# Optimization experiments

Measured on AMD Instinct MI355X. Metric: run time of the kernel, lower is better.

Reference implementation:

```python
import jax, jax.numpy as jnp
import numpy as np

N = 100000          # total nodes
E = 3200000         # total edges (avg degree 32)
B = 100             # num graphs
NPG = N // B        # nodes per graph (uniform -> to_dense_batch is a reshape)
D_IN, D_H, D_E, N_CLS = 128, 64, 32, 10


def setup_inputs() -> dict:
    key = jax.random.key(0)
    ks = jax.random.split(key, 12)
    x = jax.random.normal(ks[0], (N, D_IN), jnp.float32)
    # edges strictly within each graph: offset by graph block
    epg = E // B
    offs = (jnp.arange(E, dtype=jnp.int32) // epg) * NPG
    src = jax.random.randint(ks[1], (E,), 0, NPG, jnp.int32) + offs
    dst = jax.random.randint(ks[2], (E,), 0, NPG, jnp.int32) + offs
    edge_index = jnp.stack([src, dst])
    batch = jnp.repeat(jnp.arange(B, dtype=jnp.int32), NPG)

    def glorot(k, fi, fo):
        return jax.random.normal(k, (fi, fo), jnp.float32) * (1.0 / np.sqrt(fi))

    return {
        "x": x, "edge_index": edge_index, "batch": batch,
        "W_a1": glorot(ks[3], D_IN, D_H), "b_a1": jnp.zeros((D_H,), jnp.float32),
        "W_a2": glorot(ks[4], D_H, D_E),  "b_a2": jnp.zeros((D_E,), jnp.float32),
        "W_x1": glorot(ks[5], D_IN, D_H), "b_x1": jnp.zeros((D_H,), jnp.float32),
        "W_x2": glorot(ks[6], D_H, D_E),  "b_x2": jnp.zeros((D_E,), jnp.float32),
        "W_lin": glorot(ks[7], D_E * D_E, N_CLS),
        "b_lin": jnp.zeros((N_CLS,), jnp.float32),
    }


def _gcn(x, W, b, src, dst, n):
    """PyG GCNConv(improved=True): sym-norm with self-loop weight 2."""
    h = x @ W                                                   # [n, out]
    deg = jax.ops.segment_sum(jnp.ones_like(dst, h.dtype), dst, n) + 2.0
    dinv = jax.lax.rsqrt(deg)                                   # [n]
    coef = dinv[src] * dinv[dst]                                # [E]
    agg = jax.ops.segment_sum(h[src] * coef[:, None], dst, n)   # gather-scatter
    agg = agg + (2.0 * dinv * dinv)[:, None] * h                # self-loop term
    return agg + b


def _segment_softmax(v, seg, nseg):
    m = jax.ops.segment_max(v, seg, nseg)
    e = jnp.exp(v - m[seg])
    s = jax.ops.segment_sum(e, seg, nseg)
    return e / s[seg]


def reference(x, edge_index, batch, W_a1, b_a1, W_a2, b_a2,
              W_x1, b_x1, W_x2, b_x2, W_lin, b_lin):
    src, dst = edge_index[0], edge_index[1]
    n = x.shape[0]
    a1 = jax.nn.relu(_gcn(x, W_a1, b_a1, src, dst, n))
    a2 = _segment_softmax(_gcn(a1, W_a2, b_a2, src, dst, n), batch, B)
    x1 = jax.nn.relu(_gcn(x, W_x1, b_x1, src, dst, n))
    x2 = jax.nn.relu(_gcn(x1, W_x2, b_x2, src, dst, n))
    # uniform graph sizes -> to_dense_batch is a reshape (no padding needed)
    a_b = a2.reshape(B, NPG, D_E)
    x_b = x2.reshape(B, NPG, D_E)
    prods = jnp.einsum('bne,bnf->bef', a_b, x_b)   # bmm(a^T, x): [B, D_E, D_E]
    flat = prods.reshape(B, D_E * D_E)
    return jax.nn.softmax(flat @ W_lin + b_lin, axis=-1)
```

## Files before the change

### kernel.cpp

```cpp
#include <hip/hip_runtime.h>
#include <hip/hip_bf16.h>
#include <hip/hip_fp16.h>

#define N_NODES 100000
#define N_EDGES 3200000
#define NB      100
#define NPG     1000
#define EPG     32000
#define DIN     128
#define DH      64
#define DE      32
#define NCLS    10
#define CNT_BLOCKS  832
#define SORT_BLOCKS 416


typedef _Float16 h2_t __attribute__((ext_vector_type(2)));
typedef _Float16 h8_t __attribute__((ext_vector_type(8)));
typedef float    f4_t __attribute__((ext_vector_type(4)));

__device__ __forceinline__ float dot2f(unsigned a, unsigned b, float c) {
#if __has_builtin(__builtin_amdgcn_fdot2)
    return __builtin_amdgcn_fdot2(__builtin_bit_cast(h2_t, a),
                                  __builtin_bit_cast(h2_t, b), c, false);
#else
    float d;
    asm("v_dot2_f32_f16 %0, %1, %2, %3" : "=v"(d) : "v"(a), "v"(b), "v"(c));
    return d;
#endif
}

#define DOT8(rA, rB, dv)                                                        \
    acc[0] = dot2f(__builtin_amdgcn_perm(rB.x, rA.x, 0x05040100u), dv, acc[0]); \
    acc[1] = dot2f(__builtin_amdgcn_perm(rB.x, rA.x, 0x07060302u), dv, acc[1]); \
    acc[2] = dot2f(__builtin_amdgcn_perm(rB.y, rA.y, 0x05040100u), dv, acc[2]); \
    acc[3] = dot2f(__builtin_amdgcn_perm(rB.y, rA.y, 0x07060302u), dv, acc[3]); \
    acc[4] = dot2f(__builtin_amdgcn_perm(rB.z, rA.z, 0x05040100u), dv, acc[4]); \
    acc[5] = dot2f(__builtin_amdgcn_perm(rB.z, rA.z, 0x07060302u), dv, acc[5]); \
    acc[6] = dot2f(__builtin_amdgcn_perm(rB.w, rA.w, 0x05040100u), dv, acc[6]); \
    acc[7] = dot2f(__builtin_amdgcn_perm(rB.w, rA.w, 0x07060302u), dv, acc[7]);

__device__ __forceinline__ unsigned fenc(float f) {
    unsigned u = __float_as_uint(f);
    return u ^ (unsigned)(((int)u >> 31) | (int)0x80000000);
}
__device__ __forceinline__ float fdec(unsigned key) {
    return (key & 0x80000000u) ? __uint_as_float(key ^ 0x80000000u)
                               : __uint_as_float(~key);
}


__global__ __launch_bounds__(256) void k_cnt(const int* __restrict__ dst,
                                             int* __restrict__ cnt8) {
    __shared__ int cnt[NPG];
    int slice = blockIdx.x >> 3;
    int g = (blockIdx.x & 7) + 8 * (slice % 13);
    int sub = slice / 13;
    if (g >= NB) return;
    int t = threadIdx.x;
    for (int i = t; i < NPG; i += 256) cnt[i] = 0;
    __syncthreads();
    int ebase = g * EPG + sub * 4000, nbase = g * NPG;
    for (int i = t; i < 4000; i += 256)
        atomicAdd(&cnt[dst[ebase + i] - nbase], 1);
    __syncthreads();
    for (int i = t; i < NPG; i += 256)
        cnt8[sub * N_NODES + nbase + i] = cnt[i];
}


__global__ __launch_bounds__(1024) void k_scan(const int* __restrict__ cnt8,
                                               int* __restrict__ rowptr,
                                               float* __restrict__ dinv,
                                               unsigned short* __restrict__ dh16) {
    __shared__ int sm[1024];
    int g = (blockIdx.x & 7) + 8 * (blockIdx.x >> 3);
    if (g >= NB) return;
    int t = threadIdx.x;
    int nbase = g * NPG, ebase = g * EPG;
    int v = 0;
    if (t < NPG) {
        #pragma unroll
        for (int s8 = 0; s8 < 8; s8++) v += cnt8[s8 * N_NODES + nbase + t];
        float dv = rsqrtf((float)v + 2.0f);
        dinv[nbase + t] = dv;
        dh16[nbase + t] = __half_as_ushort(__float2half_rn(dv));
    }
    sm[t] = v;
    __syncthreads();
    for (int off = 1; off < 1024; off <<= 1) {
        int xx = (t >= off) ? sm[t - off] : 0;
        __syncthreads();
        sm[t] += xx;
        __syncthreads();
    }
    if (t < NPG)
        rowptr[nbase + t] = ebase + sm[t] - v;
    if (g == NB - 1 && t == 0) rowptr[N_NODES] = N_EDGES;
}


union SharedSG {
    struct {
        int cur[256];
        unsigned buf[10000];
    } sc;
    struct {
        __align__(16) unsigned short wt[16384];
    } ge;
};

__global__ __launch_bounds__(1024) void k_sg(const int* __restrict__ src,
                                             const int* __restrict__ dst,
                                             const float* __restrict__ x,
                                             const float* __restrict__ Wa,
                                             const float* __restrict__ Wx,
                                             const int* __restrict__ rowptr,
                                             const unsigned short* __restrict__ dh16,
                                             unsigned int* __restrict__ esrc,
                                             unsigned short* __restrict__ h16) {
    __shared__ SharedSG S;
    int t = threadIdx.x;
    if (blockIdx.x < SORT_BLOCKS) {
        int xcd = blockIdx.x & 7, slot = blockIdx.x >> 3;
        int g = xcd + 8 * (slot % 13);
        int q = slot / 13;
        if (g >= NB) return;
        int nbase = g * NPG, ebase = g * EPG;
        int n0 = q * 250;
        int base0 = rowptr[nbase + n0];
        int cap = rowptr[nbase + n0 + 250] - base0;
        if (t < 250)
            S.sc.cur[t] = rowptr[nbase + n0 + t] - base0;
        __syncthreads();
        for (int i = t; i < EPG; i += 1024) {
            int d = dst[ebase + i] - nbase - n0;
            if ((unsigned)d < 250u) {
                int s = src[ebase + i];
                int pos = atomicAdd(&S.sc.cur[d], 1);
                S.sc.buf[pos] = ((unsigned)(s - nbase) * 16) |
                                ((unsigned)dh16[s] << 16);
            }
        }
        __syncthreads();
        for (int i = t; i < cap; i += 1024)
            esrc[base0 + i] = S.sc.buf[i];
    } else {
        int b2 = blockIdx.x - SORT_BLOCKS;
        int xcd = b2 & 7, slot = b2 >> 3;
        int g = xcd + 8 * (slot >> 2);
        int chunk = slot & 3;
        if (g >= NB) return;
        int row0 = g * NPG + chunk * 250;
        {
            int cc = t & 127, kg = t >> 7;
            const float* Wp = (cc < 64) ? &Wa[cc] : &Wx[cc - 64];
            #pragma unroll
            for (int j = 0; j < 4; j++) {
                int k0 = kg * 16 + j * 4;
                union { __half h[4]; uint2 u; } pk;
                #pragma unroll
                for (int m = 0; m < 4; m++)
                    pk.h[m] = __float2half_rn(Wp[(k0 + m) * 64]);
                int byte = cc * 256 + ((2 * k0) ^ ((cc & 7) << 4));
                *(uint2*)((char*)S.ge.wt + byte) = pk.u;
            }
        }
        __syncthreads();
        int w = t >> 6, l = t & 63;
        int lr = l & 15, kq = l >> 4;
        int rowA = row0 + w * 16 + lr;
        int rA = rowA < N_NODES ? rowA : N_NODES - 1;
        const float* xr = &x[(size_t)rA * 128];
        h8_t a[4];
        #pragma unroll
        for (int kc = 0; kc < 4; kc++) {
            float4 lo = *(const float4*)&xr[kc * 32 + kq * 8];
            float4 hi = *(const float4*)&xr[kc * 32 + kq * 8 + 4];
            h8_t av;
            av[0] = (_Float16)lo.x; av[1] = (_Float16)lo.y;
            av[2] = (_Float16)lo.z; av[3] = (_Float16)lo.w;
            av[4] = (_Float16)hi.x; av[5] = (_Float16)hi.y;
            av[6] = (_Float16)hi.z; av[7] = (_Float16)hi.w;
            a[kc] = av;
        }
        f4_t acc[8] = {};
        #pragma unroll
        for (int kc = 0; kc < 4; kc++) {
            #pragma unroll
            for (int n = 0; n < 8; n++) {
                int cc = n * 16 + lr;
                int byte = cc * 256 + (((kc * 32 + kq * 8) * 2) ^ ((cc & 7) << 4));
                h8_t bf = *(h8_t*)((char*)S.ge.wt + byte);
                acc[n] = __builtin_amdgcn_mfma_f32_16x16x32_f16(a[kc], bf, acc[n], 0, 0, 0);
            }
        }
        int rowD = row0 + w * 16 + kq * 4;
        #pragma unroll
        for (int n = 0; n < 8; n++) {
            #pragma unroll
            for (int j = 0; j < 4; j++) {
                int r = rowD + j;
                if (r < N_NODES)
                    h16[(size_t)r * 128 + n * 16 + lr] =
                        __half_as_ushort(__float2half_rn(acc[n][j]));
            }
        }
    }
}


__global__ __launch_bounds__(256) void k_agg128(const unsigned short* __restrict__ h16,
                                                const int* __restrict__ rowptr,
                                                const unsigned int* __restrict__ esrc,
                                                const float* __restrict__ dinv,
                                                const float* __restrict__ ba,
                                                const float* __restrict__ bx,
                                                unsigned short* __restrict__ outB16) {
    int xcd = blockIdx.x & 7, slot = blockIdx.x >> 3;
    int gi = slot / 63, chunk = slot - gi * 63;
    int g = xcd + 8 * gi;
    if (g >= NB) return;
    int grp = threadIdx.x >> 4;
    int cl  = threadIdx.x & 15;
    int nl  = chunk * 16 + grp;
    int valid = nl < NPG;
    int nlc = valid ? nl : NPG - 1;
    int wid = g * NPG + nlc;
    const uint4* hg4 = (const uint4*)(h16 + (size_t)g * NPG * 128);
    float acc[8] = {};
    union U8 { uint4 u; __half h[8]; };
    int e0 = rowptr[wid];
    int e1 = valid ? rowptr[wid + 1] : e0;
    int e = e0;
    for (; e + 8 <= e1; e += 8) {
        unsigned pv0 = esrc[e + 0], pv1 = esrc[e + 1];
        unsigned pv2 = esrc[e + 2], pv3 = esrc[e + 3];
        unsigned pv4 = esrc[e + 4], pv5 = esrc[e + 5];
        unsigned pv6 = esrc[e + 6], pv7 = esrc[e + 7];
        uint4 r0 = hg4[(pv0 & 0xffffu) + cl];
        uint4 r1 = hg4[(pv1 & 0xffffu) + cl];
        uint4 r2 = hg4[(pv2 & 0xffffu) + cl];
        uint4 r3 = hg4[(pv3 & 0xffffu) + cl];
        uint4 r4 = hg4[(pv4 & 0xffffu) + cl];
        uint4 r5 = hg4[(pv5 & 0xffffu) + cl];
        uint4 r6 = hg4[(pv6 & 0xffffu) + cl];
        uint4 r7 = hg4[(pv7 & 0xffffu) + cl];
        unsigned dA = __builtin_amdgcn_perm(pv1, pv0, 0x07060302u);
        unsigned dB = __builtin_amdgcn_perm(pv3, pv2, 0x07060302u);
        unsigned dC = __builtin_amdgcn_perm(pv5, pv4, 0x07060302u);
        unsigned dD = __builtin_amdgcn_perm(pv7, pv6, 0x07060302u);
        DOT8(r0, r1, dA);
        DOT8(r2, r3, dB);
        DOT8(r4, r5, dC);
        DOT8(r6, r7, dD);
    }
    for (; e + 2 <= e1; e += 2) {
        unsigned pv0 = esrc[e], pv1 = esrc[e + 1];
        uint4 r0 = hg4[(pv0 & 0xffffu) + cl];
        uint4 r1 = hg4[(pv1 & 0xffffu) + cl];
        unsigned dA = __builtin_amdgcn_perm(pv1, pv0, 0x07060302u);
        DOT8(r0, r1, dA);
    }
    if (e < e1) {
        unsigned pv = esrc[e];
        uint4 r = hg4[(pv & 0xffffu) + cl];
        unsigned dA = pv >> 16;
        DOT8(r, r, dA);
    }
    float di = dinv[wid];
    float sw = 2.0f * di * di;
    U8 hv; hv.u = hg4[nlc * 16 + cl];
    int cl8 = cl * 8;
    const float* bb = (cl8 < 64) ? &ba[cl8] : &bx[cl8 - 64];
    union { __half2 h2[4]; uint4 q; } pk;
    #pragma unroll
    for (int k = 0; k < 4; k++) {
        float ox = fmaxf(di * acc[2 * k]     + sw * __half2float(hv.h[2 * k])     + bb[2 * k],     0.0f);
        float oy = fmaxf(di * acc[2 * k + 1] + sw * __half2float(hv.h[2 * k + 1]) + bb[2 * k + 1], 0.0f);
        pk.h2[k] = __floats2half2_rn(ox, oy);
    }
    if (valid)
        *(uint4*)&outB16[(size_t)wid * 128 + cl8] = pk.q;
}


__global__ __launch_bounds__(256) void k_agg64(const unsigned short* __restrict__ g16,
                                               const int* __restrict__ rowptr,
                                               const unsigned int* __restrict__ esrc,
                                               const float* __restrict__ dinv,
                                               const float* __restrict__ ba2,
                                               const float* __restrict__ bx2,
                                               float* __restrict__ s2,
                                               float* __restrict__ pmax) {
    __shared__ unsigned pm[32];
    int xcd = blockIdx.x & 7, slot = blockIdx.x >> 3;
    int gi = slot >> 5, chunk = slot & 31;
    int g = xcd + 8 * gi;
    if (g >= NB) return;
    int t = threadIdx.x;
    if (t < 32) pm[t] = 0u;
    __syncthreads();
    int grp = t >> 3;
    int cl  = t & 7;
    int nl  = chunk * 32 + grp;
    int valid = nl < NPG;
    int nlc = valid ? nl : NPG - 1;
    int wid = g * NPG + nlc;
    const uint4* gg4 = (const uint4*)(g16 + (size_t)g * NPG * 64);
    float acc[8] = {};
    union U8 { uint4 u; __half h[8]; };
    int e0 = rowptr[wid];
    int e1 = valid ? rowptr[wid + 1] : e0;
    int e = e0;
    for (; e + 8 <= e1; e += 8) {
        unsigned pv0 = esrc[e + 0], pv1 = esrc[e + 1];
        unsigned pv2 = esrc[e + 2], pv3 = esrc[e + 3];
        unsigned pv4 = esrc[e + 4], pv5 = esrc[e + 5];
        unsigned pv6 = esrc[e + 6], pv7 = esrc[e + 7];
        uint4 r0 = gg4[((pv0 & 0xffffu) >> 1) + cl];
        uint4 r1 = gg4[((pv1 & 0xffffu) >> 1) + cl];
        uint4 r2 = gg4[((pv2 & 0xffffu) >> 1) + cl];
        uint4 r3 = gg4[((pv3 & 0xffffu) >> 1) + cl];
        uint4 r4 = gg4[((pv4 & 0xffffu) >> 1) + cl];
        uint4 r5 = gg4[((pv5 & 0xffffu) >> 1) + cl];
        uint4 r6 = gg4[((pv6 & 0xffffu) >> 1) + cl];
        uint4 r7 = gg4[((pv7 & 0xffffu) >> 1) + cl];
        unsigned dA = __builtin_amdgcn_perm(pv1, pv0, 0x07060302u);
        unsigned dB = __builtin_amdgcn_perm(pv3, pv2, 0x07060302u);
        unsigned dC = __builtin_amdgcn_perm(pv5, pv4, 0x07060302u);
        unsigned dD = __builtin_amdgcn_perm(pv7, pv6, 0x07060302u);
        DOT8(r0, r1, dA);
        DOT8(r2, r3, dB);
        DOT8(r4, r5, dC);
        DOT8(r6, r7, dD);
    }
    for (; e + 2 <= e1; e += 2) {
        unsigned pv0 = esrc[e], pv1 = esrc[e + 1];
        uint4 r0 = gg4[((pv0 & 0xffffu) >> 1) + cl];
        uint4 r1 = gg4[((pv1 & 0xffffu) >> 1) + cl];
        unsigned dA = __builtin_amdgcn_perm(pv1, pv0, 0x07060302u);
        DOT8(r0, r1, dA);
    }
    if (e < e1) {
        unsigned pv = esrc[e];
        uint4 r = gg4[((pv & 0xffffu) >> 1) + cl];
        unsigned dA = pv >> 16;
        DOT8(r, r, dA);
    }
    float di = dinv[wid];
    float sw = 2.0f * di * di;
    U8 hv; hv.u = gg4[nlc * 8 + cl];
    int cl8 = cl * 8;
    float o[8];
    #pragma unroll
    for (int k = 0; k < 8; k++)
        o[k] = di * acc[k] + sw * __half2float(hv.h[k]);
    if (cl8 < 32) {
        #pragma unroll
        for (int k = 0; k < 8; k++) o[k] += ba2[cl8 + k];
    } else {
        #pragma unroll
        for (int k = 0; k < 8; k++) o[k] = fmaxf(o[k] + bx2[cl8 - 32 + k], 0.0f);
    }
    if (valid) {
        *(float4*)&s2[(size_t)wid * 64 + cl8]     = make_float4(o[0], o[1], o[2], o[3]);
        *(float4*)&s2[(size_t)wid * 64 + cl8 + 4] = make_float4(o[4], o[5], o[6], o[7]);
    }
    if (valid && cl < 4) {
        #pragma unroll
        for (int k = 0; k < 8; k++)
            atomicMax(&pm[cl8 + k], fenc(o[k]));
    }
    __syncthreads();
    if (t < 32)
        pmax[((size_t)g * 32 + chunk) * 32 + t] = fdec(pm[t]);
}


__global__ __launch_bounds__(256) void k_gemm2(const unsigned short* __restrict__ Bm16,
                                               const float* __restrict__ Wa2,
                                               const float* __restrict__ Wx2,
                                               unsigned short* __restrict__ g16) {
    __shared__ __align__(16) unsigned short wt2[8192];
    int xcd = blockIdx.x & 7, slot = blockIdx.x >> 3;
    int g = xcd + 8 * (slot >> 4);
    int chunk = slot & 15;
    if (g >= NB) return;
    int row0 = g * NPG + chunk * 64;
    int t = threadIdx.x;
    {
        int cc = t & 63, kg = t >> 6;
        #pragma unroll
        for (int j = 0; j < 8; j++) {
            int k0 = kg * 32 + j * 4;
            union { __half h[4]; uint2 u; } pk;
            #pragma unroll
            for (int m = 0; m < 4; m++) {
                int k = k0 + m;
                float v;
                if (cc < 32) v = (k < 64)  ? Wa2[k * 32 + cc] : 0.0f;
                else         v = (k >= 64) ? Wx2[(k - 64) * 32 + (cc - 32)] : 0.0f;
                pk.h[m] = __float2half_rn(v);
            }
            int byte = cc * 256 + ((2 * k0) ^ ((cc & 7) << 4));
            *(uint2*)((char*)wt2 + byte) = pk.u;
        }
    }
    __syncthreads();
    int w = t >> 6, l = t & 63;
    int lr = l & 15, kq = l >> 4;
    int rowA = row0 + w * 16 + lr;
    int rA = rowA < N_NODES ? rowA : N_NODES - 1;
    const unsigned short* xr = &Bm16[(size_t)rA * 128];
    h8_t a[4];
    #pragma unroll
    for (int kc = 0; kc < 4; kc++)
        a[kc] = *(const h8_t*)&xr[kc * 32 + kq * 8];
    f4_t acc[4] = {};
    #pragma unroll
    for (int kc = 0; kc < 4; kc++) {
        #pragma unroll
        for (int n = 0; n < 4; n++) {
            int cc = n * 16 + lr;
            int byte = cc * 256 + (((kc * 32 + kq * 8) * 2) ^ ((cc & 7) << 4));
            h8_t bf = *(h8_t*)((char*)wt2 + byte);
            acc[n] = __builtin_amdgcn_mfma_f32_16x16x32_f16(a[kc], bf, acc[n], 0, 0, 0);
        }
    }
    int rowD = row0 + w * 16 + kq * 4;
    #pragma unroll
    for (int n = 0; n < 4; n++) {
        #pragma unroll
        for (int j = 0; j < 4; j++) {
            int r = rowD + j;
            if (r < N_NODES)
                g16[(size_t)r * 64 + n * 16 + lr] =
                    __half_as_ushort(__float2half_rn(acc[n][j]));
        }
    }
}


__global__ __launch_bounds__(256) void k_pool(const float* __restrict__ s2,
                                              const float* __restrict__ pmax,
                                              float* __restrict__ psum,
                                              float* __restrict__ prods) {
    __shared__ float ta[25][32];
    __shared__ float tx[25][32];
    __shared__ float gm[32];
    int xcd = blockIdx.x & 7, slot = blockIdx.x >> 3;
    int g = xcd + 8 * (slot >> 3);
    int ch = slot & 7;
    if (g >= NB) return;
    int t = threadIdx.x;
    if (t < 32) {
        float m = -1e30f;
        for (int j = 0; j < 32; j++)
            m = fmaxf(m, pmax[((size_t)g * 32 + j) * 32 + t]);
        gm[t] = m;
    }
    int e  = t >> 3;
    int f4 = t & 7;
    float a0 = 0.f, a1 = 0.f, a2 = 0.f, a3 = 0.f;
    float csum = 0.f;
    int base = g * NPG + ch * 125;
    for (int n0 = 0; n0 < 125; n0 += 25) {
        __syncthreads();
        for (int i = t; i < 25 * 16; i += 256) {
            int r = i >> 4, c4 = i & 15;
            float4 v = *(const float4*)&s2[(size_t)(base + n0 + r) * 64 + c4 * 4];
            if (c4 < 8) {
                int cb = c4 * 4;
                v.x = __expf(v.x - gm[cb + 0]);
                v.y = __expf(v.y - gm[cb + 1]);
                v.z = __expf(v.z - gm[cb + 2]);
                v.w = __expf(v.w - gm[cb + 3]);
                *(float4*)&ta[r][cb] = v;
            } else {
                *(float4*)&tx[r][(c4 - 8) * 4] = v;
            }
        }
        __syncthreads();
        if (t < 32) {
            #pragma unroll 5
            for (int r = 0; r < 25; r++) csum += ta[r][t];
        }
        #pragma unroll 5
        for (int n = 0; n < 25; n++) {
            float a   = ta[n][e];
            float4 xv = *(float4*)&tx[n][f4 * 4];
            a0 += a * xv.x; a1 += a * xv.y; a2 += a * xv.z; a3 += a * xv.w;
        }
    }
    if (t < 32)
        psum[((size_t)g * 8 + ch) * 32 + t] = csum;
    *(float4*)&prods[((size_t)(g * 8 + ch)) * 1024 + e * 32 + f4 * 4] =
        make_float4(a0, a1, a2, a3);
}


__global__ __launch_bounds__(256) void k_head(const float* __restrict__ prods,
                                              const float* __restrict__ psum,
                                              const float* __restrict__ Wlin,
                                              const float* __restrict__ blin,
                                              float* __restrict__ out) {
    __shared__ float red[4][NCLS];
    __shared__ float sinvv[32];
    int g = (blockIdx.x & 7) + 8 * (blockIdx.x >> 3);
    if (g >= NB) return;
    int t = threadIdx.x;
    if (t < 32) {
        float s = 0.f;
        for (int q = 0; q < 8; q++) s += psum[((size_t)g * 8 + q) * 32 + t];
        sinvv[t] = 1.0f / s;
    }
    __syncthreads();
    float p[NCLS];
    for (int c = 0; c < NCLS; c++) p[c] = 0.0f;
    const float* pg = &prods[(size_t)g * 8 * 1024];
    for (int j = 0; j < 4; j++) {
        int k = t * 4 + j;
        int e = k >> 5;
        float v = 0.0f;
        #pragma unroll
        for (int q = 0; q < 8; q++) v += pg[q * 1024 + k];
        v *= sinvv[e];
        const float* wrow = &Wlin[k * NCLS];
        for (int c = 0; c < NCLS; c++) p[c] += v * wrow[c];
    }
    for (int off = 32; off > 0; off >>= 1)
        for (int c = 0; c < NCLS; c++) p[c] += __shfl_down(p[c], off, 64);
    int wave = t >> 6, lane = t & 63;
    if (lane == 0)
        for (int c = 0; c < NCLS; c++) red[wave][c] = p[c];
    __syncthreads();
    if (t == 0) {
        float logits[NCLS]; float mx = -1e30f;
        for (int c = 0; c < NCLS; c++) {
            logits[c] = red[0][c] + red[1][c] + red[2][c] + red[3][c] + blin[c];
            mx = fmaxf(mx, logits[c]);
        }
        float s = 0.0f;
        for (int c = 0; c < NCLS; c++) { logits[c] = expf(logits[c] - mx); s += logits[c]; }
        float inv = 1.0f / s;
        for (int c = 0; c < NCLS; c++) out[g * NCLS + c] = logits[c] * inv;
    }
}


extern "C" void kernel_launch(void* const* d_in, const int* in_sizes, int n_in,
                              void* d_out, int out_size, void* d_ws, size_t ws_size,
                              hipStream_t stream) {
    const float* x    = (const float*)d_in[0];
    const int*   ei   = (const int*)d_in[1];
    const float* Wa1  = (const float*)d_in[3];
    const float* ba1  = (const float*)d_in[4];
    const float* Wa2  = (const float*)d_in[5];
    const float* ba2  = (const float*)d_in[6];
    const float* Wx1  = (const float*)d_in[7];
    const float* bx1  = (const float*)d_in[8];
    const float* Wx2  = (const float*)d_in[9];
    const float* bx2  = (const float*)d_in[10];
    const float* Wlin = (const float*)d_in[11];
    const float* blin = (const float*)d_in[12];
    float* out = (float*)d_out;

    char* w = (char*)d_ws;
    auto alloc = [&](size_t bytes) -> void* {
        void* p = (void*)w;
        w += (bytes + 255) & ~(size_t)255;
        return p;
    };
    int*            rowptr = (int*)alloc((N_NODES + 1) * sizeof(int));
    int*            cnt8   = (int*)alloc((size_t)8 * N_NODES * sizeof(int));
    float*          dinv   = (float*)alloc(N_NODES * sizeof(float));
    unsigned short* dh16   = (unsigned short*)alloc(N_NODES * sizeof(unsigned short));
    unsigned int*   esrc   = (unsigned int*)alloc((size_t)N_EDGES * sizeof(unsigned int));
    float*          pmax   = (float*)alloc((size_t)NB * 32 * 32 * sizeof(float));
    float*          psum   = (float*)alloc((size_t)NB * 8 * 32 * sizeof(float));
    float*          prods  = (float*)alloc((size_t)NB * 8 * 1024 * sizeof(float));
    unsigned short* h16    = (unsigned short*)alloc((size_t)N_NODES * 128 * sizeof(unsigned short));
    unsigned short* b16    = (unsigned short*)alloc((size_t)N_NODES * 128 * sizeof(unsigned short));
    unsigned short* g16    = (unsigned short*)alloc((size_t)N_NODES * 64 * sizeof(unsigned short));
    float*          s2     = (float*)alloc((size_t)N_NODES * 64 * sizeof(float));

    const int* srcp = ei;
    const int* dstp = ei + N_EDGES;

    k_cnt<<<CNT_BLOCKS, 256, 0, stream>>>(dstp, cnt8);
    k_scan<<<8 * 13, 1024, 0, stream>>>(cnt8, rowptr, dinv, dh16);
    k_sg<<<SORT_BLOCKS + 8 * 13 * 4, 1024, 0, stream>>>(srcp, dstp, x, Wa1, Wx1,
                                                        rowptr, dh16, esrc, h16);
    k_agg128<<<8 * 13 * 63, 256, 0, stream>>>(h16, rowptr, esrc, dinv, ba1, bx1, b16);
    k_gemm2<<<8 * 13 * 16, 256, 0, stream>>>(b16, Wa2, Wx2, g16);
    k_agg64<<<8 * 13 * 32, 256, 0, stream>>>(g16, rowptr, esrc, dinv, ba2, bx2, s2, pmax);
    k_pool<<<8 * 13 * 8, 256, 0, stream>>>(s2, pmax, psum, prods);
    k_head<<<8 * 13, 256, 0, stream>>>(prods, psum, Wlin, blin, out);
}
```

Before: 288.4 us.

## Replace first-layer gather aggregation with dense per-graph SpMM on MFMA

Stores the first-layer projected features transposed per graph (channel-major). It replaces the per-node edge gather with a kernel that builds a dense 64x128 fp16 adjacency tile in shared memory for each K-slice of source nodes, then multiplies it with the feature tile using MFMA. The aim is to swap irregular gathered loads for dense tensor-core work, since each graph has only 1000 nodes. In exchange, every block rescans its edge lists 8 times, the adjacency accumulates in fp16, and the epilogue makes strided scalar reads and writes.

```diff
diff --git a/kernel.cpp b/kernel.cpp
--- a/kernel.cpp
+++ b/kernel.cpp
@@ -118,7 +118,7 @@
                                              const int* __restrict__ rowptr,
                                              const unsigned short* __restrict__ dh16,
                                              unsigned int* __restrict__ esrc,
-                                             unsigned short* __restrict__ h16) {
+                                             unsigned short* __restrict__ h16t) {
     __shared__ SharedSG S;
     int t = threadIdx.x;
     if (blockIdx.x < SORT_BLOCKS) {
@@ -195,93 +195,125 @@
                 acc[n] = __builtin_amdgcn_mfma_f32_16x16x32_f16(a[kc], bf, acc[n], 0, 0, 0);
             }
         }
-        int rowD = row0 + w * 16 + kq * 4;
+        int nodeLoc = chunk * 250 + w * 16 + kq * 4;
         #pragma unroll
         for (int n = 0; n < 8; n++) {
+            int ch = n * 16 + lr;
+            unsigned short* hrow = h16t + ((size_t)g * 128 + ch) * 1000;
             #pragma unroll
             for (int j = 0; j < 4; j++) {
-                int r = rowD + j;
-                if (r < N_NODES)
-                    h16[(size_t)r * 128 + n * 16 + lr] =
-                        __half_as_ushort(__float2half_rn(acc[n][j]));
-            }
-        }
-    }
-}
-
-
-__global__ __launch_bounds__(256) void k_agg128(const unsigned short* __restrict__ h16,
-                                                const int* __restrict__ rowptr,
-                                                const unsigned int* __restrict__ esrc,
-                                                const float* __restrict__ dinv,
-                                                const float* __restrict__ ba,
-                                                const float* __restrict__ bx,
-                                                unsigned short* __restrict__ outB16) {
+                int nl = nodeLoc + j;
+                if (nl < NPG)
+                    hrow[nl] = __half_as_ushort(__float2half_rn(acc[n][j]));
+            }
+        }
+    }
+}
+
+
+__global__ __launch_bounds__(256) void k_spmm128(const unsigned short* __restrict__ h16t,
+                                                 const int* __restrict__ rowptr,
+                                                 const unsigned int* __restrict__ esrc,
+                                                 const float* __restrict__ dinv,
+                                                 const float* __restrict__ ba,
+                                                 const float* __restrict__ bx,
+                                                 unsigned short* __restrict__ outB16) {
+    __shared__ __align__(16) unsigned short As[8192];
+    __shared__ __align__(16) unsigned short Bt[16384];
     int xcd = blockIdx.x & 7, slot = blockIdx.x >> 3;
-    int gi = slot / 63, chunk = slot - gi * 63;
+    int gi = slot >> 4, chunk = slot & 15;
     int g = xcd + 8 * gi;
     if (g >= NB) return;
-    int grp = threadIdx.x >> 4;
-    int cl  = threadIdx.x & 15;
-    int nl  = chunk * 16 + grp;
-    int valid = nl < NPG;
-    int nlc = valid ? nl : NPG - 1;
-    int wid = g * NPG + nlc;
-    const uint4* hg4 = (const uint4*)(h16 + (size_t)g * NPG * 128);
-    float acc[8] = {};
-    union U8 { uint4 u; __half h[8]; };
-    int e0 = rowptr[wid];
-    int e1 = valid ? rowptr[wid + 1] : e0;
-    int e = e0;
-    for (; e + 8 <= e1; e += 8) {
-        unsigned pv0 = esrc[e + 0], pv1 = esrc[e + 1];
-        unsigned pv2 = esrc[e + 2], pv3 = esrc[e + 3];
-        unsigned pv4 = esrc[e + 4], pv5 = esrc[e + 5];
-        unsigned pv6 = esrc[e + 6], pv7 = esrc[e + 7];
-        uint4 r0 = hg4[(pv0 & 0xffffu) + cl];
-        uint4 r1 = hg4[(pv1 & 0xffffu) + cl];
-        uint4 r2 = hg4[(pv2 & 0xffffu) + cl];
-        uint4 r3 = hg4[(pv3 & 0xffffu) + cl];
-        uint4 r4 = hg4[(pv4 & 0xffffu) + cl];
-        uint4 r5 = hg4[(pv5 & 0xffffu) + cl];
-        uint4 r6 = hg4[(pv6 & 0xffffu) + cl];
-        uint4 r7 = hg4[(pv7 & 0xffffu) + cl];
-        unsigned dA = __builtin_amdgcn_perm(pv1, pv0, 0x07060302u);
-        unsigned dB = __builtin_amdgcn_perm(pv3, pv2, 0x07060302u);
-        unsigned dC = __builtin_amdgcn_perm(pv5, pv4, 0x07060302u);
-        unsigned dD = __builtin_amdgcn_perm(pv7, pv6, 0x07060302u);
-        DOT8(r0, r1, dA);
-        DOT8(r2, r3, dB);
-        DOT8(r4, r5, dC);
-        DOT8(r6, r7, dD);
-    }
-    for (; e + 2 <= e1; e += 2) {
-        unsigned pv0 = esrc[e], pv1 = esrc[e + 1];
-        uint4 r0 = hg4[(pv0 & 0xffffu) + cl];
-        uint4 r1 = hg4[(pv1 & 0xffffu) + cl];
-        unsigned dA = __builtin_amdgcn_perm(pv1, pv0, 0x07060302u);
-        DOT8(r0, r1, dA);
-    }
-    if (e < e1) {
-        unsigned pv = esrc[e];
-        uint4 r = hg4[(pv & 0xffffu) + cl];
-        unsigned dA = pv >> 16;
-        DOT8(r, r, dA);
-    }
-    float di = dinv[wid];
-    float sw = 2.0f * di * di;
-    U8 hv; hv.u = hg4[nlc * 16 + cl];
-    int cl8 = cl * 8;
-    const float* bb = (cl8 < 64) ? &ba[cl8] : &bx[cl8 - 64];
-    union { __half2 h2[4]; uint4 q; } pk;
+    int t = threadIdx.x;
+    int w = t >> 6, l = t & 63, lr = l & 15, kq = l >> 4;
+    int n0 = chunk * 64;
+    int eb0 = 0, eb1 = 0;
+    if (t < 64) {
+        int nl = n0 + t;
+        if (nl < NPG) {
+            int wid = g * NPG + nl;
+            eb0 = rowptr[wid];
+            eb1 = rowptr[wid + 1];
+        }
+    }
+    const unsigned short* hb = h16t + (size_t)g * 128 * 1000;
+    f4_t acc[8] = {};
+    for (int sk = 0; sk < 8; sk++) {
+        __syncthreads();
+        {
+            uint4 z = make_uint4(0, 0, 0, 0);
+            #pragma unroll
+            for (int i = 0; i < 4; i++)
+                *(uint4*)((char*)As + t * 64 + i * 16) = z;
+        }
+        {
+            int tch = t >> 1, th = t & 1;
+            #pragma unroll
+            for (int i = 0; i < 8; i++) {
+                int kl = th * 64 + i * 8;
+                int nb = sk * 128 + kl;
+                int nsrc = (nb + 8 <= NPG) ? nb : (NPG - 8);
+                uint4 v = *(const uint4*)(hb + (size_t)tch * 1000 + nsrc);
+                *(uint4*)((char*)Bt + tch * 256 + ((2 * kl) ^ ((tch & 7) << 4))) = v;
+            }
+        }
+        __syncthreads();
+        if (t < 64) {
+            int slo = sk << 7;
+            int e = eb0;
+            for (; e + 4 <= eb1; e += 4) {
+                unsigned q0 = esrc[e], q1 = esrc[e + 1];
+                unsigned q2 = esrc[e + 2], q3 = esrc[e + 3];
+                #pragma unroll
+                for (int j = 0; j < 4; j++) {
+                    unsigned rec = (j == 0) ? q0 : (j == 1) ? q1 : (j == 2) ? q2 : q3;
+                    int sl = (int)((rec & 0xffffu) >> 4) - slo;
+                    if ((unsigned)sl < 128u) {
+                        __half* ap = (__half*)((char*)As + t * 256 + ((2 * sl) ^ ((t & 7) << 4)));
+                        *ap = __hadd(*ap, __ushort_as_half((unsigned short)(rec >> 16)));
+                    }
+                }
+            }
+            for (; e < eb1; e++) {
+                unsigned rec = esrc[e];
+                int sl = (int)((rec & 0xffffu) >> 4) - slo;
+                if ((unsigned)sl < 128u) {
+                    __half* ap = (__half*)((char*)As + t * 256 + ((2 * sl) ^ ((t & 7) << 4)));
+                    *ap = __hadd(*ap, __ushort_as_half((unsigned short)(rec >> 16)));
+                }
+            }
+        }
+        __syncthreads();
+        #pragma unroll
+        for (int kk = 0; kk < 4; kk++) {
+            int row = w * 16 + lr;
+            h8_t a = *(h8_t*)((char*)As + row * 256 + ((kk * 64 + kq * 16) ^ ((row & 7) << 4)));
+            #pragma unroll
+            for (int n = 0; n < 8; n++) {
+                int ch = n * 16 + lr;
+                h8_t b = *(h8_t*)((char*)Bt + ch * 256 + ((kk * 64 + kq * 16) ^ ((ch & 7) << 4)));
+                acc[n] = __builtin_amdgcn_mfma_f32_16x16x32_f16(a, b, acc[n], 0, 0, 0);
+            }
+        }
+    }
+    int nodeBase = n0 + w * 16 + kq * 4;
     #pragma unroll
-    for (int k = 0; k < 4; k++) {
-        float ox = fmaxf(di * acc[2 * k]     + sw * __half2float(hv.h[2 * k])     + bb[2 * k],     0.0f);
-        float oy = fmaxf(di * acc[2 * k + 1] + sw * __half2float(hv.h[2 * k + 1]) + bb[2 * k + 1], 0.0f);
-        pk.h2[k] = __floats2half2_rn(ox, oy);
-    }
-    if (valid)
-        *(uint4*)&outB16[(size_t)wid * 128 + cl8] = pk.q;
+    for (int j = 0; j < 4; j++) {
+        int nl = nodeBase + j;
+        if (nl < NPG) {
+            int wid = g * NPG + nl;
+            float di = dinv[wid];
+            float sw = 2.0f * di * di;
+            #pragma unroll
+            for (int n = 0; n < 8; n++) {
+                int ch = n * 16 + lr;
+                float hs = __half2float(__ushort_as_half(hb[(size_t)ch * 1000 + nl]));
+                float bbv = (ch < 64) ? ba[ch] : bx[ch - 64];
+                float o = fmaxf(di * acc[n][j] + sw * hs + bbv, 0.0f);
+                outB16[(size_t)wid * 128 + ch] = __half_as_ushort(__float2half_rn(o));
+            }
+        }
+    }
 }
 
 
@@ -580,7 +612,7 @@
     float*          pmax   = (float*)alloc((size_t)NB * 32 * 32 * sizeof(float));
     float*          psum   = (float*)alloc((size_t)NB * 8 * 32 * sizeof(float));
     float*          prods  = (float*)alloc((size_t)NB * 8 * 1024 * sizeof(float));
-    unsigned short* h16    = (unsigned short*)alloc((size_t)N_NODES * 128 * sizeof(unsigned short));
+    unsigned short* h16t   = (unsigned short*)alloc((size_t)N_NODES * 128 * sizeof(unsigned short));
     unsigned short* b16    = (unsigned short*)alloc((size_t)N_NODES * 128 * sizeof(unsigned short));
     unsigned short* g16    = (unsigned short*)alloc((size_t)N_NODES * 64 * sizeof(unsigned short));
     float*          s2     = (float*)alloc((size_t)N_NODES * 64 * sizeof(float));
@@ -591,8 +623,8 @@
     k_cnt<<<CNT_BLOCKS, 256, 0, stream>>>(dstp, cnt8);
     k_scan<<<8 * 13, 1024, 0, stream>>>(cnt8, rowptr, dinv, dh16);
     k_sg<<<SORT_BLOCKS + 8 * 13 * 4, 1024, 0, stream>>>(srcp, dstp, x, Wa1, Wx1,
-                                                        rowptr, dh16, esrc, h16);
-    k_agg128<<<8 * 13 * 63, 256, 0, stream>>>(h16, rowptr, esrc, dinv, ba1, bx1, b16);
+                                                        rowptr, dh16, esrc, h16t);
+    k_spmm128<<<8 * 13 * 16, 256, 0, stream>>>(h16t, rowptr, esrc, dinv, ba1, bx1, b16);
     k_gemm2<<<8 * 13 * 16, 256, 0, stream>>>(b16, Wa2, Wx2, g16);
     k_agg64<<<8 * 13 * 32, 256, 0, stream>>>(g16, rowptr, esrc, dinv, ba2, bx2, s2, pmax);
     k_pool<<<8 * 13 * 8, 256, 0, stream>>>(s2, pmax, psum, prods);
```

Measured after the change: 434.0 us. 1.5x slower.

## Fuse second-layer GEMM into first aggregation kernel via shared-memory MFMA

Applied to the files above, without the earlier changes.

The layer-2 weight multiply (128->64 block-diagonal) now happens inside k_agg128. Each block stages its 16 aggregated rows in swizzled LDS and runs MFMA against the fp16 weights, also staged in LDS, then writes g16 directly. This removes the k_gemm2 launch and the write and re-read of the 25.6 MB b16 intermediate. In exchange, every one of the ~6500 blocks now converts the full weight matrix to fp16 in LDS, and LDS use and the extra barrier may lower occupancy of the latency-bound gather kernel.

```diff
diff --git a/kernel.cpp b/kernel.cpp
--- a/kernel.cpp
+++ b/kernel.cpp
@@ -216,13 +216,36 @@
                                                 const float* __restrict__ dinv,
                                                 const float* __restrict__ ba,
                                                 const float* __restrict__ bx,
-                                                unsigned short* __restrict__ outB16) {
+                                                const float* __restrict__ Wa2,
+                                                const float* __restrict__ Wx2,
+                                                unsigned short* __restrict__ g16) {
+    __shared__ __align__(16) unsigned short wt2[8192];
+    __shared__ __align__(16) unsigned short bs[2048];
     int xcd = blockIdx.x & 7, slot = blockIdx.x >> 3;
     int gi = slot / 63, chunk = slot - gi * 63;
     int g = xcd + 8 * gi;
     if (g >= NB) return;
-    int grp = threadIdx.x >> 4;
-    int cl  = threadIdx.x & 15;
+    int t = threadIdx.x;
+    {
+        int cc = t & 63, kg = t >> 6;
+        #pragma unroll
+        for (int j = 0; j < 8; j++) {
+            int k0 = kg * 32 + j * 4;
+            union { __half h[4]; uint2 u; } pk;
+            #pragma unroll
+            for (int m = 0; m < 4; m++) {
+                int k = k0 + m;
+                float v;
+                if (cc < 32) v = (k < 64)  ? Wa2[k * 32 + cc] : 0.0f;
+                else         v = (k >= 64) ? Wx2[(k - 64) * 32 + (cc - 32)] : 0.0f;
+                pk.h[m] = __float2half_rn(v);
+            }
+            int byte = cc * 256 + ((2 * k0) ^ ((cc & 7) << 4));
+            *(uint2*)((char*)wt2 + byte) = pk.u;
+        }
+    }
+    int grp = t >> 4;
+    int cl  = t & 15;
     int nl  = chunk * 16 + grp;
     int valid = nl < NPG;
     int nlc = valid ? nl : NPG - 1;
@@ -268,20 +291,41 @@
         unsigned dA = pv >> 16;
         DOT8(r, r, dA);
     }
-    float di = dinv[wid];
-    float sw = 2.0f * di * di;
-    U8 hv; hv.u = hg4[nlc * 16 + cl];
-    int cl8 = cl * 8;
-    const float* bb = (cl8 < 64) ? &ba[cl8] : &bx[cl8 - 64];
-    union { __half2 h2[4]; uint4 q; } pk;
-    #pragma unroll
-    for (int k = 0; k < 4; k++) {
-        float ox = fmaxf(di * acc[2 * k]     + sw * __half2float(hv.h[2 * k])     + bb[2 * k],     0.0f);
-        float oy = fmaxf(di * acc[2 * k + 1] + sw * __half2float(hv.h[2 * k + 1]) + bb[2 * k + 1], 0.0f);
-        pk.h2[k] = __floats2half2_rn(ox, oy);
-    }
-    if (valid)
-        *(uint4*)&outB16[(size_t)wid * 128 + cl8] = pk.q;
+    {
+        float di = dinv[wid];
+        float sw = 2.0f * di * di;
+        U8 hv; hv.u = hg4[nlc * 16 + cl];
+        int cl8 = cl * 8;
+        const float* bb = (cl8 < 64) ? &ba[cl8] : &bx[cl8 - 64];
+        union { __half h[8]; uint4 q; } pk;
+        #pragma unroll
+        for (int k = 0; k < 8; k++) {
+            float o = fmaxf(di * acc[k] + sw * __half2float(hv.h[k]) + bb[k], 0.0f);
+            pk.h[k] = valid ? __float2half_rn(o) : __float2half_rn(0.0f);
+        }
+        *(uint4*)((char*)bs + grp * 256 + ((cl * 16) ^ ((grp & 7) << 4))) = pk.q;
+    }
+    __syncthreads();
+    {
+        int w = t >> 6, l = t & 63;
+        int lr = l & 15, kq = l >> 4;
+        f4_t acc2 = {0.0f, 0.0f, 0.0f, 0.0f};
+        #pragma unroll
+        for (int kc = 0; kc < 4; kc++) {
+            int kb = (kc * 32 + kq * 8) * 2;
+            h8_t a = *(h8_t*)((char*)bs + lr * 256 + (kb ^ ((lr & 7) << 4)));
+            int cc = w * 16 + lr;
+            h8_t bfr = *(h8_t*)((char*)wt2 + cc * 256 + (kb ^ ((cc & 7) << 4)));
+            acc2 = __builtin_amdgcn_mfma_f32_16x16x32_f16(a, bfr, acc2, 0, 0, 0);
+        }
+        #pragma unroll
+        for (int j = 0; j < 4; j++) {
+            int nl2 = chunk * 16 + 4 * kq + j;
+            if (nl2 < NPG)
+                g16[((size_t)(g * NPG + nl2)) * 64 + w * 16 + lr] =
+                    __half_as_ushort(__float2half_rn(acc2[j]));
+        }
+    }
 }
 
 
@@ -378,70 +422,6 @@
 }
 
 
-__global__ __launch_bounds__(256) void k_gemm2(const unsigned short* __restrict__ Bm16,
-                                               const float* __restrict__ Wa2,
-                                               const float* __restrict__ Wx2,
-                                               unsigned short* __restrict__ g16) {
-    __shared__ __align__(16) unsigned short wt2[8192];
-    int xcd = blockIdx.x & 7, slot = blockIdx.x >> 3;
-    int g = xcd + 8 * (slot >> 4);
-    int chunk = slot & 15;
-    if (g >= NB) return;
-    int row0 = g * NPG + chunk * 64;
-    int t = threadIdx.x;
-    {
-        int cc = t & 63, kg = t >> 6;
-        #pragma unroll
-        for (int j = 0; j < 8; j++) {
-            int k0 = kg * 32 + j * 4;
-            union { __half h[4]; uint2 u; } pk;
-            #pragma unroll
-            for (int m = 0; m < 4; m++) {
-                int k = k0 + m;
-                float v;
-                if (cc < 32) v = (k < 64)  ? Wa2[k * 32 + cc] : 0.0f;
-                else         v = (k >= 64) ? Wx2[(k - 64) * 32 + (cc - 32)] : 0.0f;
-                pk.h[m] = __float2half_rn(v);
-            }
-            int byte = cc * 256 + ((2 * k0) ^ ((cc & 7) << 4));
-            *(uint2*)((char*)wt2 + byte) = pk.u;
-        }
-    }
-    __syncthreads();
-    int w = t >> 6, l = t & 63;
-    int lr = l & 15, kq = l >> 4;
-    int rowA = row0 + w * 16 + lr;
-    int rA = rowA < N_NODES ? rowA : N_NODES - 1;
-    const unsigned short* xr = &Bm16[(size_t)rA * 128];
-    h8_t a[4];
-    #pragma unroll
-    for (int kc = 0; kc < 4; kc++)
-        a[kc] = *(const h8_t*)&xr[kc * 32 + kq * 8];
-    f4_t acc[4] = {};
-    #pragma unroll
-    for (int kc = 0; kc < 4; kc++) {
-        #pragma unroll
-        for (int n = 0; n < 4; n++) {
-            int cc = n * 16 + lr;
-            int byte = cc * 256 + (((kc * 32 + kq * 8) * 2) ^ ((cc & 7) << 4));
-            h8_t bf = *(h8_t*)((char*)wt2 + byte);
-            acc[n] = __builtin_amdgcn_mfma_f32_16x16x32_f16(a[kc], bf, acc[n], 0, 0, 0);
-        }
-    }
-    int rowD = row0 + w * 16 + kq * 4;
-    #pragma unroll
-    for (int n = 0; n < 4; n++) {
-        #pragma unroll
-        for (int j = 0; j < 4; j++) {
-            int r = rowD + j;
-            if (r < N_NODES)
-                g16[(size_t)r * 64 + n * 16 + lr] =
-                    __half_as_ushort(__float2half_rn(acc[n][j]));
-        }
-    }
-}
-
-
 __global__ __launch_bounds__(256) void k_pool(const float* __restrict__ s2,
                                               const float* __restrict__ pmax,
                                               float* __restrict__ psum,
@@ -581,7 +561,6 @@
     float*          psum   = (float*)alloc((size_t)NB * 8 * 32 * sizeof(float));
     float*          prods  = (float*)alloc((size_t)NB * 8 * 1024 * sizeof(float));
     unsigned short* h16    = (unsigned short*)alloc((size_t)N_NODES * 128 * sizeof(unsigned short));
-    unsigned short* b16    = (unsigned short*)alloc((size_t)N_NODES * 128 * sizeof(unsigned short));
     unsigned short* g16    = (unsigned short*)alloc((size_t)N_NODES * 64 * sizeof(unsigned short));
     float*          s2     = (float*)alloc((size_t)N_NODES * 64 * sizeof(float));
 
@@ -592,8 +571,8 @@
     k_scan<<<8 * 13, 1024, 0, stream>>>(cnt8, rowptr, dinv, dh16);
     k_sg<<<SORT_BLOCKS + 8 * 13 * 4, 1024, 0, stream>>>(srcp, dstp, x, Wa1, Wx1,
                                                         rowptr, dh16, esrc, h16);
-    k_agg128<<<8 * 13 * 63, 256, 0, stream>>>(h16, rowptr, esrc, dinv, ba1, bx1, b16);
-    k_gemm2<<<8 * 13 * 16, 256, 0, stream>>>(b16, Wa2, Wx2, g16);
+    k_agg128<<<8 * 13 * 63, 256, 0, stream>>>(h16, rowptr, esrc, dinv, ba1, bx1,
+                                              Wa2, Wx2, g16);
     k_agg64<<<8 * 13 * 32, 256, 0, stream>>>(g16, rowptr, esrc, dinv, ba2, bx2, s2, pmax);
     k_pool<<<8 * 13 * 8, 256, 0, stream>>>(s2, pmax, psum, prods);
     k_head<<<8 * 13, 256, 0, stream>>>(prods, psum, Wlin, blin, out);
```

After: 290.8 us. No clear change (+0.8%).
